# Kernel optimization log

Hardware: AMD Instinct MI355X
Metric: run time of the kernel (lower is better)

## Reference

```python
import jax, jax.numpy as jnp
import numpy as np

N_NODES = 50000
N_EDGES = 800000
N_POS = 200000
NFEAT = 512
NHID = 256


def setup_inputs() -> dict:
    key = jax.random.key(0)
    ks = jax.random.split(key, 7)
    x = jax.random.normal(ks[0], (N_NODES, NFEAT), dtype=jnp.float32)
    edge_index = jax.random.randint(ks[1], (2, N_EDGES), 0, N_NODES, dtype=jnp.int32)
    edge_weight = jax.random.uniform(ks[2], (N_EDGES,), dtype=jnp.float32)
    pos_edge_index = jax.random.randint(ks[3], (2, N_POS), 0, N_NODES, dtype=jnp.int32)
    W1 = jax.random.normal(ks[4], (NFEAT, NHID), dtype=jnp.float32) * (1.0 / np.sqrt(NFEAT))
    W2 = jax.random.normal(ks[5], (NHID, NHID), dtype=jnp.float32) * (1.0 / np.sqrt(NHID))
    Wlin = jax.random.normal(ks[6], (2 * NHID, 2), dtype=jnp.float32) * (1.0 / np.sqrt(2 * NHID))
    return {"x": x, "edge_index": edge_index, "edge_weight": edge_weight,
            "pos_edge_index": pos_edge_index, "W1": W1, "W2": W2, "Wlin": Wlin}


def _gcn_conv(h, W, src, dst, edge_weight, num_nodes):
    # GCNConv(normalize=False, add_self_loops=False, bias=False):
    # out[dst] += edge_weight * (h @ W)[src]
    h = h @ W  # [N, out]
    msg = edge_weight[:, None] * h[src]  # [E, out]
    return jax.ops.segment_sum(msg, dst, num_segments=num_nodes)


def reference(x, edge_index, edge_weight, pos_edge_index, W1, W2, Wlin):
    src, dst = edge_index[0], edge_index[1]
    n = x.shape[0]
    z = _gcn_conv(x, W1, src, dst, edge_weight, n)
    z = jax.nn.relu(z)
    z = _gcn_conv(z, W2, src, dst, edge_weight, n)
    # decode: gather endpoints, concat, linear (no bias)
    h = jnp.concatenate([z[pos_edge_index[0]], z[pos_edge_index[1]]], axis=1)  # [P, 2*nhid]
    return h @ Wlin  # [P, 2]
```

## Files before the change

### kernel.cpp

```cpp
#include <hip/hip_runtime.h>

#define NHID 256
#define NFEAT 512

using short8  = __attribute__((ext_vector_type(8))) short;
using float8  = __attribute__((ext_vector_type(8))) float;
using f32x4   = __attribute__((ext_vector_type(4))) float;

__device__ __forceinline__ float b2f(unsigned short u) {
    union { float f; unsigned v; } c;
    c.v = ((unsigned)u) << 16;
    return c.f;
}
__device__ __forceinline__ unsigned short f2b(float f) {
    union { float f; unsigned u; } c;
    c.f = f;
    unsigned r = c.u + 0x7fffu + ((c.u >> 16) & 1u);
    return (unsigned short)(r >> 16);
}
__device__ __forceinline__ unsigned short f2h(float f) {
    union { _Float16 h; unsigned short u; } c;
    c.h = (_Float16)f;
    return c.u;
}
__device__ __forceinline__ float h2f(unsigned short u) {
    union { _Float16 h; unsigned short u; } c;
    c.u = u;
    return (float)c.h;
}

__device__ __forceinline__ void gload16(const void* gsrc, void* lds) {
    __builtin_amdgcn_global_load_lds((const __attribute__((address_space(1))) unsigned int*)gsrc,
                                     (__attribute__((address_space(3))) unsigned int*)lds,
                                     16, 0, 0);
}

__global__ __launch_bounds__(256) void prep_all(const float* __restrict__ W1,
                                                const float* __restrict__ W2,
                                                const float* __restrict__ Wlin,
                                                unsigned short* __restrict__ F1,
                                                float* __restrict__ WP,
                                                int* __restrict__ cursor, int M) {
    int i = blockIdx.x * blockDim.x + threadIdx.x;
    const int T1 = NFEAT * NHID;
    if (i < T1) {
        int j = i & 7, l = (i >> 3) & 63, cb = (i >> 9) & 15, t = i >> 13;
        int n = cb * 16 + (l & 15);
        int k = t * 32 + ((l >> 4) << 3) + j;
        F1[i] = f2b(W1[k * NHID + n]);
    } else if (i < T1 + NHID * 4) {
        int i3 = i - T1;
        int k = i3 >> 2, j = i3 & 3;
        const int base = (j >= 2) ? NHID : 0;
        const int col = j & 1;
        float acc = 0.f;
        for (int n = 0; n < NHID; ++n)
            acc += W2[k * NHID + n] * Wlin[(base + n) * 2 + col];
        WP[k * 4 + j] = acc;
    } else {
        int j = i - T1 - NHID * 4;
        if (j < M) cursor[j] = 0;
    }
}

__global__ __launch_bounds__(256) void gemm1_pipe(const float* __restrict__ x,
                                                  const unsigned short* __restrict__ F1,
                                                  unsigned short* __restrict__ C, int M) {
    __shared__ float As[3][64 * 32];
    __shared__ unsigned short Bs[3][8192];
    const int tid = threadIdx.x;
    const int lane = tid & 63;
    const int wc = tid >> 6;
    const int brow = blockIdx.x * 64;
    const int lrow = lane & 15;
    const int lq = lane >> 4;
    const int nt = NFEAT / 32;

    int ar0 = brow + wc * 16 + (lane >> 3);
    int ar1 = ar0 + 8;
    if (ar0 >= M) ar0 = M - 1;
    if (ar1 >= M) ar1 = M - 1;
    const int aswz = ((lane & 7) ^ (lane >> 3)) * 4;
    const float* ag0 = x + (size_t)ar0 * NFEAT + aswz;
    const float* ag1 = x + (size_t)ar1 * NFEAT + aswz;
    const unsigned short* bsrc = F1 + (wc * 4) * 512 + lane * 8;

    f32x4 acc[4][4] = {};

#define STAGE1(bf, t) do { \
        gload16(ag0 + (t) * 32, (char*)&As[bf][0] + wc * 2048); \
        gload16(ag1 + (t) * 32, (char*)&As[bf][0] + wc * 2048 + 1024); \
        const unsigned short* bs_ = bsrc + (t) * 8192; \
        gload16(bs_ + 0 * 512, &Bs[bf][(wc * 4 + 0) * 512]); \
        gload16(bs_ + 1 * 512, &Bs[bf][(wc * 4 + 1) * 512]); \
        gload16(bs_ + 2 * 512, &Bs[bf][(wc * 4 + 2) * 512]); \
        gload16(bs_ + 3 * 512, &Bs[bf][(wc * 4 + 3) * 512]); \
    } while (0)

    STAGE1(0, 0);
    STAGE1(1, 1);

#pragma unroll
    for (int t = 0; t < 16; ++t) {
        if (t < nt - 1) asm volatile("s_waitcnt vmcnt(6)" ::: "memory");
        else            asm volatile("s_waitcnt vmcnt(0)" ::: "memory");
        __builtin_amdgcn_s_barrier();
        __builtin_amdgcn_sched_barrier(0);
        if (t + 2 < nt) STAGE1((t + 2) % 3, t + 2);

        const int rb = t % 3;
        short8 a[4], b[4];
#pragma unroll
        for (int m = 0; m < 4; ++m) {
            int row = m * 16 + lrow;
            const char* base = (const char*)&As[rb][0] + row * 128;
            int sw = (row & 7) << 4;
            float4 f0 = *(const float4*)(base + ((lq * 32) ^ sw));
            float4 f1 = *(const float4*)(base + ((lq * 32 + 16) ^ sw));
            short8 v;
            v[0] = (short)f2b(f0.x); v[1] = (short)f2b(f0.y);
            v[2] = (short)f2b(f0.z); v[3] = (short)f2b(f0.w);
            v[4] = (short)f2b(f1.x); v[5] = (short)f2b(f1.y);
            v[6] = (short)f2b(f1.z); v[7] = (short)f2b(f1.w);
            a[m] = v;
        }
#pragma unroll
        for (int n = 0; n < 4; ++n)
            b[n] = *(const short8*)(&Bs[rb][(wc * 4 + n) * 512 + lane * 8]);
#pragma unroll
        for (int m = 0; m < 4; ++m)
#pragma unroll
            for (int n = 0; n < 4; ++n)
                acc[m][n] = __builtin_amdgcn_mfma_f32_16x16x32_bf16(a[m], b[n], acc[m][n], 0, 0, 0);
    }
#undef STAGE1

#pragma unroll
    for (int m = 0; m < 4; ++m)
#pragma unroll
        for (int r = 0; r < 4; ++r) {
            int row = brow + m * 16 + (lane >> 4) * 4 + r;
            if (row < M) {
#pragma unroll
                for (int n = 0; n < 4; ++n) {
                    int col = wc * 64 + n * 16 + (lane & 15);
                    C[(size_t)row * NHID + col] = f2b(acc[m][n][r]);
                }
            }
        }
}

__global__ __launch_bounds__(256) void hist_part(const int* __restrict__ dst,
                                                 int* __restrict__ counts,
                                                 int E, int span, int M) {
    const int g = blockIdx.x & 7;
    const int rank = blockIdx.x >> 3;
    const int nrank = gridDim.x >> 3;
    const int lo = g * span;
    const int hi = min(lo + span, M);
    for (int e = rank * blockDim.x + threadIdx.x; e < E; e += nrank * blockDim.x) {
        int d = dst[e];
        if (d >= lo && d < hi) atomicAdd(&counts[d], 1);
    }
}

__global__ __launch_bounds__(1024) void scan_local(const int* __restrict__ counts,
                                                   int* __restrict__ local,
                                                   int* __restrict__ blocksums, int n) {
    __shared__ int s[1024];
    const int tid = threadIdx.x;
    const int idx = blockIdx.x * 1024 + tid;
    int v = (idx < n) ? counts[idx] : 0;
    s[tid] = v;
    __syncthreads();
    for (int off = 1; off < 1024; off <<= 1) {
        int t = (tid >= off) ? s[tid - off] : 0;
        __syncthreads();
        s[tid] += t;
        __syncthreads();
    }
    if (idx < n) local[idx] = s[tid] - v;
    if (tid == 1023) blocksums[blockIdx.x] = s[1023];
}

__global__ __launch_bounds__(1024) void scan_sums(int* __restrict__ blocksums, int nb) {
    __shared__ int s[1024];
    const int tid = threadIdx.x;
    int v = (tid < nb) ? blocksums[tid] : 0;
    s[tid] = v;
    __syncthreads();
    for (int off = 1; off < 1024; off <<= 1) {
        int t = (tid >= off) ? s[tid - off] : 0;
        __syncthreads();
        s[tid] += t;
        __syncthreads();
    }
    if (tid < nb) blocksums[tid] = s[tid] - v;
}

__global__ __launch_bounds__(256) void scan_finalize(int* __restrict__ offsets,
                                                     int* __restrict__ cursor,
                                                     const int* __restrict__ blockoffs,
                                                     int n, int total) {
    int idx = blockIdx.x * blockDim.x + threadIdx.x;
    if (idx < n) {
        int o = offsets[idx] + blockoffs[idx >> 10];
        offsets[idx] = o;
        cursor[idx] = o;
    }
    if (idx == 0) offsets[n] = total;
}

__global__ __launch_bounds__(256) void sort_edges_part(const int* __restrict__ src,
                                                       const int* __restrict__ dst,
                                                       const float* __restrict__ w,
                                                       int* __restrict__ cursor,
                                                       unsigned* __restrict__ pk,
                                                       int E, int span, int M) {
    const int g = blockIdx.x & 7;
    const int rank = blockIdx.x >> 3;
    const int nrank = gridDim.x >> 3;
    const int lo = g * span;
    const int hi = min(lo + span, M);
    for (int e = rank * blockDim.x + threadIdx.x; e < E; e += nrank * blockDim.x) {
        int d = dst[e];
        if (d >= lo && d < hi) {
            int pos = atomicAdd(&cursor[d], 1);
            pk[pos] = ((unsigned)f2h(w[e]) << 16) | (unsigned)src[e];
        }
    }
}

__global__ __launch_bounds__(256) void gather1_proj(const unsigned short* __restrict__ h,
                                                    const int* __restrict__ offsets,
                                                    const unsigned* __restrict__ pk,
                                                    const float* __restrict__ WP,
                                                    float4* __restrict__ y4, int N) {
    const int lane = threadIdx.x & 63;
    const int wid = threadIdx.x >> 6;
    const int node = blockIdx.x * 4 + wid;
    if (node >= N) return;

    float wp[4][4];
#pragma unroll
    for (int i = 0; i < 4; ++i) {
        float4 r = ((const float4*)WP)[lane * 4 + i];
        wp[i][0] = r.x; wp[i][1] = r.y; wp[i][2] = r.z; wp[i][3] = r.w;
    }

    const int s0 = offsets[node];
    const int s1 = offsets[node + 1];
    float a0 = 0.f, a1 = 0.f, a2 = 0.f, a3 = 0.f;
    int i = s0;
    for (; i + 4 <= s1; i += 4) {
        unsigned qA = pk[i], qB = pk[i + 1], qC = pk[i + 2], qD = pk[i + 3];
        float wA = h2f(qA >> 16), wB = h2f(qB >> 16), wC = h2f(qC >> 16), wD = h2f(qD >> 16);
        ushort4 vA = ((const ushort4*)(h + (size_t)(qA & 0xffffu) * NHID))[lane];
        ushort4 vB = ((const ushort4*)(h + (size_t)(qB & 0xffffu) * NHID))[lane];
        ushort4 vC = ((const ushort4*)(h + (size_t)(qC & 0xffffu) * NHID))[lane];
        ushort4 vD = ((const ushort4*)(h + (size_t)(qD & 0xffffu) * NHID))[lane];
        a0 += wA * b2f(vA.x) + wB * b2f(vB.x) + wC * b2f(vC.x) + wD * b2f(vD.x);
        a1 += wA * b2f(vA.y) + wB * b2f(vB.y) + wC * b2f(vC.y) + wD * b2f(vD.y);
        a2 += wA * b2f(vA.z) + wB * b2f(vB.z) + wC * b2f(vC.z) + wD * b2f(vD.z);
        a3 += wA * b2f(vA.w) + wB * b2f(vB.w) + wC * b2f(vC.w) + wD * b2f(vD.w);
    }
    for (; i < s1; ++i) {
        unsigned q = pk[i];
        float ww = h2f(q >> 16);
        ushort4 v = ((const ushort4*)(h + (size_t)(q & 0xffffu) * NHID))[lane];
        a0 += ww * b2f(v.x);
        a1 += ww * b2f(v.y);
        a2 += ww * b2f(v.z);
        a3 += ww * b2f(v.w);
    }
    a0 = fmaxf(a0, 0.f); a1 = fmaxf(a1, 0.f);
    a2 = fmaxf(a2, 0.f); a3 = fmaxf(a3, 0.f);

    float t0 = a0 * wp[0][0] + a1 * wp[1][0] + a2 * wp[2][0] + a3 * wp[3][0];
    float t1 = a0 * wp[0][1] + a1 * wp[1][1] + a2 * wp[2][1] + a3 * wp[3][1];
    float t2 = a0 * wp[0][2] + a1 * wp[1][2] + a2 * wp[2][2] + a3 * wp[3][2];
    float t3 = a0 * wp[0][3] + a1 * wp[1][3] + a2 * wp[2][3] + a3 * wp[3][3];
#pragma unroll
    for (int off = 32; off > 0; off >>= 1) {
        t0 += __shfl_down(t0, off);
        t1 += __shfl_down(t1, off);
        t2 += __shfl_down(t2, off);
        t3 += __shfl_down(t3, off);
    }
    if (lane == 0) y4[node] = {t0, t1, t2, t3};
}

__global__ __launch_bounds__(256) void gather2_small(const float4* __restrict__ y4,
                                                     const int* __restrict__ offsets,
                                                     const unsigned* __restrict__ pk,
                                                     float2* __restrict__ za,
                                                     float2* __restrict__ zb, int N) {
    const int lane = threadIdx.x & 63;
    const int wid = threadIdx.x >> 6;
    const int grp = lane >> 4;
    const int slot = lane & 15;
    const int node = blockIdx.x * 16 + wid * 4 + grp;
    if (node >= N) return;

    const int s0 = offsets[node];
    const int s1 = offsets[node + 1];
    float x0 = 0.f, x1 = 0.f, x2 = 0.f, x3 = 0.f;
    for (int i = s0 + slot; i < s1; i += 16) {
        unsigned q = pk[i];
        float ww = h2f(q >> 16);
        float4 v = y4[q & 0xffffu];
        x0 += ww * v.x; x1 += ww * v.y; x2 += ww * v.z; x3 += ww * v.w;
    }
#pragma unroll
    for (int off = 8; off > 0; off >>= 1) {
        x0 += __shfl_xor(x0, off);
        x1 += __shfl_xor(x1, off);
        x2 += __shfl_xor(x2, off);
        x3 += __shfl_xor(x3, off);
    }
    if (slot == 0) {
        za[node] = {x0, x1};
        zb[node] = {x2, x3};
    }
}

__global__ __launch_bounds__(256) void decode_pairs(const float2* __restrict__ za,
                                                    const float2* __restrict__ zb,
                                                    const int* __restrict__ ps,
                                                    const int* __restrict__ pd,
                                                    float2* __restrict__ out, int P) {
    int p = blockIdx.x * blockDim.x + threadIdx.x;
    if (p < P) {
        float2 va = za[ps[p]];
        float2 vb = zb[pd[p]];
        out[p] = {va.x + vb.x, va.y + vb.y};
    }
}

template <bool RELU>
__global__ __launch_bounds__(256) void gemm_tiled(const float* __restrict__ A,
                                                  const float* __restrict__ B,
                                                  float* __restrict__ C,
                                                  int M, int N, int K) {
    __shared__ float As[16][65];
    __shared__ float Bs[16][64];
    const int block_row = blockIdx.x * 64;
    const int block_col = blockIdx.y * 64;
    const int tid = threadIdx.x;
    const int tx = tid & 15;
    const int ty = tid >> 4;
    float c[4][4] = {};
    for (int k0 = 0; k0 < K; k0 += 16) {
#pragma unroll
        for (int i = 0; i < 4; ++i) {
            int idx = tid + i * 256;
            int kk = idx & 15;
            int m = idx >> 4;
            int row = block_row + m;
            float v = 0.f;
            if (row < M) v = A[(long)row * K + k0 + kk];
            if (RELU) v = fmaxf(v, 0.f);
            As[kk][m] = v;
        }
#pragma unroll
        for (int i = 0; i < 4; ++i) {
            int idx = tid + i * 256;
            int n = idx & 63;
            int kk = idx >> 6;
            Bs[kk][n] = B[(long)(k0 + kk) * N + block_col + n];
        }
        __syncthreads();
#pragma unroll
        for (int kk = 0; kk < 16; ++kk) {
            float a[4], b[4];
#pragma unroll
            for (int i = 0; i < 4; ++i) a[i] = As[kk][ty * 4 + i];
#pragma unroll
            for (int j = 0; j < 4; ++j) b[j] = Bs[kk][tx * 4 + j];
#pragma unroll
            for (int i = 0; i < 4; ++i)
#pragma unroll
                for (int j = 0; j < 4; ++j) c[i][j] += a[i] * b[j];
        }
        __syncthreads();
    }
#pragma unroll
    for (int i = 0; i < 4; ++i) {
        int row = block_row + ty * 4 + i;
        if (row < M) {
            float* cp = C + (long)row * N + block_col + tx * 4;
#pragma unroll
            for (int j = 0; j < 4; ++j) cp[j] = c[i][j];
        }
    }
}

__global__ __launch_bounds__(256) void scatter_conv(const float* __restrict__ h,
                                                    const int* __restrict__ src,
                                                    const int* __restrict__ dst,
                                                    const float* __restrict__ w,
                                                    float* __restrict__ z, int E) {
    const int lane = threadIdx.x & 63;
    const int wid = threadIdx.x >> 6;
    const int nwaves = (gridDim.x * blockDim.x) >> 6;
    for (int e = blockIdx.x * 4 + wid; e < E; e += nwaves) {
        int s = src[e];
        int d = dst[e];
        float ww = w[e];
        float4 v = ((const float4*)(h + (long)s * NHID))[lane];
        float* zp = z + (long)d * NHID + lane * 4;
        atomicAdd(zp + 0, ww * v.x);
        atomicAdd(zp + 1, ww * v.y);
        atomicAdd(zp + 2, ww * v.z);
        atomicAdd(zp + 3, ww * v.w);
    }
}

__global__ __launch_bounds__(256) void decode_f(const float* __restrict__ z,
                                                const int* __restrict__ ps,
                                                const int* __restrict__ pd,
                                                const float* __restrict__ Wlin,
                                                float* __restrict__ out, int P) {
    const int lane = threadIdx.x & 63;
    const int wid = threadIdx.x >> 6;
    const int nwaves = (gridDim.x * blockDim.x) >> 6;
    float wa[8], wb[8];
#pragma unroll
    for (int i = 0; i < 8; ++i) {
        wa[i] = Wlin[(lane * 4) * 2 + i];
        wb[i] = Wlin[(NHID + lane * 4) * 2 + i];
    }
    for (int p = blockIdx.x * 4 + wid; p < P; p += nwaves) {
        int a = ps[p];
        int b = pd[p];
        float4 va = ((const float4*)(z + (long)a * NHID))[lane];
        float4 vb = ((const float4*)(z + (long)b * NHID))[lane];
        float acc0 = va.x * wa[0] + va.y * wa[2] + va.z * wa[4] + va.w * wa[6]
                   + vb.x * wb[0] + vb.y * wb[2] + vb.z * wb[4] + vb.w * wb[6];
        float acc1 = va.x * wa[1] + va.y * wa[3] + va.z * wa[5] + va.w * wa[7]
                   + vb.x * wb[1] + vb.y * wb[3] + vb.z * wb[5] + vb.w * wb[7];
#pragma unroll
        for (int off = 32; off > 0; off >>= 1) {
            acc0 += __shfl_down(acc0, off);
            acc1 += __shfl_down(acc1, off);
        }
        if (lane == 0) {
            out[(long)p * 2 + 0] = acc0;
            out[(long)p * 2 + 1] = acc1;
        }
    }
}

extern "C" void kernel_launch(void* const* d_in, const int* in_sizes, int n_in,
                              void* d_out, int out_size, void* d_ws, size_t ws_size,
                              hipStream_t stream) {
    (void)n_in; (void)out_size;
    const float* x    = (const float*)d_in[0];
    const int*   ei   = (const int*)d_in[1];
    const float* ew   = (const float*)d_in[2];
    const int*   pei  = (const int*)d_in[3];
    const float* W1   = (const float*)d_in[4];
    const float* W2   = (const float*)d_in[5];
    const float* Wlin = (const float*)d_in[6];
    float* out = (float*)d_out;

    const int E = in_sizes[2];
    const int P = in_sizes[3] / 2;
    const int M = in_sizes[0] / NFEAT;

    dim3 blk(256);
    const int* src = ei;
    const int* dst = ei + E;

    unsigned short* hA = (unsigned short*)d_ws;
    unsigned short* hB = hA + (size_t)M * NHID;
    int* offsets = (int*)(hB + (size_t)M * NHID);
    int* cursor  = offsets + (M + 1);
    unsigned* pk = (unsigned*)(cursor + M);
    int* blocksums = (int*)(pk + E);
    float2* za = (float2*)(blocksums + 1024);
    float2* zb = za + M;
    const size_t need = 2 * (size_t)M * NHID * 2 + ((size_t)2 * M + 1) * 4
                      + (size_t)E * 4 + 1024 * 4 + (size_t)M * 2 * 8;

    if (ws_size >= need && M <= 65535) {
        unsigned short* F1 = (unsigned short*)d_out;
        float* WP = (float*)((char*)d_out + (size_t)NFEAT * NHID * 2);
        float4* y4 = (float4*)hB;

        const int zt = NFEAT * NHID + NHID * 4 + M;
        prep_all<<<(zt + 255) / 256, blk, 0, stream>>>(W1, W2, Wlin, F1, WP, cursor, M);

        const int span = (M + 7) / 8;
        const int nb = (M + 1023) / 1024;
        hist_part<<<2048, blk, 0, stream>>>(dst, cursor, E, span, M);
        scan_local<<<nb, 1024, 0, stream>>>(cursor, offsets, blocksums, M);
        scan_sums<<<1, 1024, 0, stream>>>(blocksums, nb);
        scan_finalize<<<(M + 255) / 256, blk, 0, stream>>>(offsets, cursor, blocksums, M, E);
        sort_edges_part<<<2048, blk, 0, stream>>>(src, dst, ew, cursor, pk, E, span, M);

        const int g = (M + 63) / 64;
        gemm1_pipe<<<g, blk, 0, stream>>>(x, F1, hA, M);
        gather1_proj<<<(M + 3) / 4, blk, 0, stream>>>(hA, offsets, pk, WP, y4, M);
        gather2_small<<<(M + 15) / 16, blk, 0, stream>>>(y4, offsets, pk, za, zb, M);
        decode_pairs<<<(P + 255) / 256, blk, 0, stream>>>(za, zb, pei, pei + P, (float2*)out, P);
    } else {
        float* bufA = (float*)d_ws;
        float* bufB = bufA + (size_t)M * NHID;
        const size_t zbytes = (size_t)M * NHID * sizeof(float);
        dim3 gemm_grid((M + 63) / 64, NHID / 64);
        gemm_tiled<false><<<gemm_grid, blk, 0, stream>>>(x, W1, bufA, M, NHID, NFEAT);
        hipMemsetAsync(bufB, 0, zbytes, stream);
        scatter_conv<<<2048, blk, 0, stream>>>(bufA, src, dst, ew, bufB, E);
        gemm_tiled<true><<<gemm_grid, blk, 0, stream>>>(bufB, W2, bufA, M, NHID, NHID);
        hipMemsetAsync(bufB, 0, zbytes, stream);
        scatter_conv<<<2048, blk, 0, stream>>>(bufA, src, dst, ew, bufB, E);
        decode_f<<<(P + 3) / 4, blk, 0, stream>>>(bufB, pei, pei + P, Wlin, out, P);
    }
}
```

Measured before the change: 204.1 us.

## Co-schedule GEMM1 halves with histogram and edge-sort kernels in fused launches

Splits the first GEMM into two halves and merges each half into the same launch as the histogram and edge-sort passes, with block-index ranges picking the role, so the compute-bound GEMM overlaps the atomic-bound CSR build. It also rewrites the GEMM main loop to double-buffer only the A tile in LDS and load the B fragments straight from global memory into registers, using __syncthreads instead of the triple-buffer waitcnt scheme. This cuts LDS use, which may raise occupancy, but B loads now sit in the critical path with less latency hiding. The CSR blocks shrink from 2048 to 1024 per launch.

Result: faster. 183.3 us (-10.2%).

```diff
diff --git a/kernel.cpp b/kernel.cpp
--- a/kernel.cpp
+++ b/kernel.cpp
@@ -63,15 +63,13 @@
     }
 }
 
-__global__ __launch_bounds__(256) void gemm1_pipe(const float* __restrict__ x,
-                                                  const unsigned short* __restrict__ F1,
-                                                  unsigned short* __restrict__ C, int M) {
-    __shared__ float As[3][64 * 32];
-    __shared__ unsigned short Bs[3][8192];
+__device__ __forceinline__ void gemm1_body(const float* __restrict__ x,
+                                           const unsigned short* __restrict__ F1,
+                                           unsigned short* __restrict__ C, int M,
+                                           int brow, char* AsRaw) {
     const int tid = threadIdx.x;
     const int lane = tid & 63;
     const int wc = tid >> 6;
-    const int brow = blockIdx.x * 64;
     const int lrow = lane & 15;
     const int lq = lane >> 4;
     const int nt = NFEAT / 32;
@@ -87,33 +85,32 @@
 
     f32x4 acc[4][4] = {};
 
-#define STAGE1(bf, t) do { \
-        gload16(ag0 + (t) * 32, (char*)&As[bf][0] + wc * 2048); \
-        gload16(ag1 + (t) * 32, (char*)&As[bf][0] + wc * 2048 + 1024); \
-        const unsigned short* bs_ = bsrc + (t) * 8192; \
-        gload16(bs_ + 0 * 512, &Bs[bf][(wc * 4 + 0) * 512]); \
-        gload16(bs_ + 1 * 512, &Bs[bf][(wc * 4 + 1) * 512]); \
-        gload16(bs_ + 2 * 512, &Bs[bf][(wc * 4 + 2) * 512]); \
-        gload16(bs_ + 3 * 512, &Bs[bf][(wc * 4 + 3) * 512]); \
-    } while (0)
-
-    STAGE1(0, 0);
-    STAGE1(1, 1);
-
+    gload16(ag0, AsRaw + wc * 2048);
+    gload16(ag1, AsRaw + wc * 2048 + 1024);
+    short8 bc0 = *(const short8*)(bsrc + 0 * 512);
+    short8 bc1 = *(const short8*)(bsrc + 1 * 512);
+    short8 bc2 = *(const short8*)(bsrc + 2 * 512);
+    short8 bc3 = *(const short8*)(bsrc + 3 * 512);
+    __syncthreads();
+
+    int p = 0;
 #pragma unroll
     for (int t = 0; t < 16; ++t) {
-        if (t < nt - 1) asm volatile("s_waitcnt vmcnt(6)" ::: "memory");
-        else            asm volatile("s_waitcnt vmcnt(0)" ::: "memory");
-        __builtin_amdgcn_s_barrier();
-        __builtin_amdgcn_sched_barrier(0);
-        if (t + 2 < nt) STAGE1((t + 2) % 3, t + 2);
-
-        const int rb = t % 3;
-        short8 a[4], b[4];
+        short8 bn0, bn1, bn2, bn3;
+        if (t + 1 < nt) {
+            gload16(ag0 + (t + 1) * 32, AsRaw + (p ^ 1) * 8192 + wc * 2048);
+            gload16(ag1 + (t + 1) * 32, AsRaw + (p ^ 1) * 8192 + wc * 2048 + 1024);
+            const unsigned short* bs_ = bsrc + (t + 1) * 8192;
+            bn0 = *(const short8*)(bs_ + 0 * 512);
+            bn1 = *(const short8*)(bs_ + 1 * 512);
+            bn2 = *(const short8*)(bs_ + 2 * 512);
+            bn3 = *(const short8*)(bs_ + 3 * 512);
+        }
+        short8 a[4];
 #pragma unroll
         for (int m = 0; m < 4; ++m) {
             int row = m * 16 + lrow;
-            const char* base = (const char*)&As[rb][0] + row * 128;
+            const char* base = AsRaw + p * 8192 + row * 128;
             int sw = (row & 7) << 4;
             float4 f0 = *(const float4*)(base + ((lq * 32) ^ sw));
             float4 f1 = *(const float4*)(base + ((lq * 32 + 16) ^ sw));
@@ -125,15 +122,16 @@
             a[m] = v;
         }
 #pragma unroll
-        for (int n = 0; n < 4; ++n)
-            b[n] = *(const short8*)(&Bs[rb][(wc * 4 + n) * 512 + lane * 8]);
-#pragma unroll
-        for (int m = 0; m < 4; ++m)
-#pragma unroll
-            for (int n = 0; n < 4; ++n)
-                acc[m][n] = __builtin_amdgcn_mfma_f32_16x16x32_bf16(a[m], b[n], acc[m][n], 0, 0, 0);
-    }
-#undef STAGE1
+        for (int m = 0; m < 4; ++m) {
+            acc[m][0] = __builtin_amdgcn_mfma_f32_16x16x32_bf16(a[m], bc0, acc[m][0], 0, 0, 0);
+            acc[m][1] = __builtin_amdgcn_mfma_f32_16x16x32_bf16(a[m], bc1, acc[m][1], 0, 0, 0);
+            acc[m][2] = __builtin_amdgcn_mfma_f32_16x16x32_bf16(a[m], bc2, acc[m][2], 0, 0, 0);
+            acc[m][3] = __builtin_amdgcn_mfma_f32_16x16x32_bf16(a[m], bc3, acc[m][3], 0, 0, 0);
+        }
+        __syncthreads();
+        p ^= 1;
+        bc0 = bn0; bc1 = bn1; bc2 = bn2; bc3 = bn3;
+    }
 
 #pragma unroll
     for (int m = 0; m < 4; ++m)
@@ -150,17 +148,59 @@
         }
 }
 
-__global__ __launch_bounds__(256) void hist_part(const int* __restrict__ dst,
-                                                 int* __restrict__ counts,
-                                                 int E, int span, int M) {
-    const int g = blockIdx.x & 7;
-    const int rank = blockIdx.x >> 3;
-    const int nrank = gridDim.x >> 3;
-    const int lo = g * span;
-    const int hi = min(lo + span, M);
-    for (int e = rank * blockDim.x + threadIdx.x; e < E; e += nrank * blockDim.x) {
-        int d = dst[e];
-        if (d >= lo && d < hi) atomicAdd(&counts[d], 1);
+__global__ __launch_bounds__(256) void fused_g1_hist(const float* __restrict__ x,
+                                                     const unsigned short* __restrict__ F1,
+                                                     unsigned short* __restrict__ C, int M,
+                                                     int gblocks,
+                                                     const int* __restrict__ dst,
+                                                     int* __restrict__ counts,
+                                                     int E, int span) {
+    __shared__ char AsRaw[2 * 8192];
+    if ((int)blockIdx.x < gblocks) {
+        gemm1_body(x, F1, C, M, blockIdx.x * 64, AsRaw);
+    } else {
+        const int rank = blockIdx.x - gblocks;
+        const int nrank = gridDim.x - gblocks;
+        const int g = rank & 7;
+        const int r8 = rank >> 3;
+        const int n8 = nrank >> 3;
+        const int lo = g * span;
+        const int hi = min(lo + span, M);
+        for (int e = r8 * blockDim.x + threadIdx.x; e < E; e += n8 * blockDim.x) {
+            int d = dst[e];
+            if (d >= lo && d < hi) atomicAdd(&counts[d], 1);
+        }
+    }
+}
+
+__global__ __launch_bounds__(256) void fused_g1_sort(const float* __restrict__ x,
+                                                     const unsigned short* __restrict__ F1,
+                                                     unsigned short* __restrict__ C, int M,
+                                                     int gblocks, int rowbase,
+                                                     const int* __restrict__ src,
+                                                     const int* __restrict__ dst,
+                                                     const float* __restrict__ w,
+                                                     int* __restrict__ cursor,
+                                                     unsigned* __restrict__ pk,
+                                                     int E, int span) {
+    __shared__ char AsRaw[2 * 8192];
+    if ((int)blockIdx.x < gblocks) {
+        gemm1_body(x, F1, C, M, (rowbase + blockIdx.x) * 64, AsRaw);
+    } else {
+        const int rank = blockIdx.x - gblocks;
+        const int nrank = gridDim.x - gblocks;
+        const int g = rank & 7;
+        const int r8 = rank >> 3;
+        const int n8 = nrank >> 3;
+        const int lo = g * span;
+        const int hi = min(lo + span, M);
+        for (int e = r8 * blockDim.x + threadIdx.x; e < E; e += n8 * blockDim.x) {
+            int d = dst[e];
+            if (d >= lo && d < hi) {
+                int pos = atomicAdd(&cursor[d], 1);
+                pk[pos] = ((unsigned)f2h(w[e]) << 16) | (unsigned)src[e];
+            }
+        }
     }
 }
 
@@ -209,26 +249,6 @@
         cursor[idx] = o;
     }
     if (idx == 0) offsets[n] = total;
-}
-
-__global__ __launch_bounds__(256) void sort_edges_part(const int* __restrict__ src,
-                                                       const int* __restrict__ dst,
-                                                       const float* __restrict__ w,
-                                                       int* __restrict__ cursor,
-                                                       unsigned* __restrict__ pk,
-                                                       int E, int span, int M) {
-    const int g = blockIdx.x & 7;
-    const int rank = blockIdx.x >> 3;
-    const int nrank = gridDim.x >> 3;
-    const int lo = g * span;
-    const int hi = min(lo + span, M);
-    for (int e = rank * blockDim.x + threadIdx.x; e < E; e += nrank * blockDim.x) {
-        int d = dst[e];
-        if (d >= lo && d < hi) {
-            int pos = atomicAdd(&cursor[d], 1);
-            pk[pos] = ((unsigned)f2h(w[e]) << 16) | (unsigned)src[e];
-        }
-    }
 }
 
 __global__ __launch_bounds__(256) void gather1_proj(const unsigned short* __restrict__ h,
@@ -493,14 +513,17 @@
 
         const int span = (M + 7) / 8;
         const int nb = (M + 1023) / 1024;
-        hist_part<<<2048, blk, 0, stream>>>(dst, cursor, E, span, M);
+        const int g = (M + 63) / 64;
+        const int g1 = g / 2;
+        const int g2 = g - g1;
+        const int CSRB = 1024;
+
+        fused_g1_hist<<<g1 + CSRB, blk, 0, stream>>>(x, F1, hA, M, g1, dst, cursor, E, span);
         scan_local<<<nb, 1024, 0, stream>>>(cursor, offsets, blocksums, M);
         scan_sums<<<1, 1024, 0, stream>>>(blocksums, nb);
         scan_finalize<<<(M + 255) / 256, blk, 0, stream>>>(offsets, cursor, blocksums, M, E);
-        sort_edges_part<<<2048, blk, 0, stream>>>(src, dst, ew, cursor, pk, E, span, M);
-
-        const int g = (M + 63) / 64;
-        gemm1_pipe<<<g, blk, 0, stream>>>(x, F1, hA, M);
+        fused_g1_sort<<<g2 + CSRB, blk, 0, stream>>>(x, F1, hA, M, g2, g1,
+                                                     src, dst, ew, cursor, pk, E, span);
         gather1_proj<<<(M + 3) / 4, blk, 0, stream>>>(hA, offsets, pk, WP, y4, M);
         gather2_small<<<(M + 15) / 16, blk, 0, stream>>>(y4, offsets, pk, za, zb, M);
         decode_pairs<<<(P + 255) / 256, blk, 0, stream>>>(za, zb, pei, pei + P, (float2*)out, P);
```
